# Optimization experiments

Hardware: AMD Instinct MI355X
Metric: run time of the kernel (lower is better)

Reference implementation:

```python
import jax, jax.numpy as jnp
from jax import lax
import numpy as np

EMBED = 20
FILTERS = 16
KSIZES = (1, 3, 5, 7, 9)
LIN_IN = 7 * len(KSIZES) * FILTERS  # 560
LIN_DIM = 64
SEQ_LENS = {'pep': 12, 'a1': 7, 'a2': 8, 'a3': 16, 'b1': 6, 'b2': 7, 'b3': 18}
BATCH = 16384


def setup_inputs() -> dict:
    key = jax.random.key(0)
    keys = jax.random.split(key, 16)
    inp = {}
    for i, (name, L) in enumerate(SEQ_LENS.items()):
        inp[name] = jax.random.normal(keys[i], (BATCH, EMBED, L), dtype=jnp.float32)
    # Conv weights: one stacked array per kernel size, [7 sequences, FILTERS, EMBED, k]
    for j, k in enumerate(KSIZES):
        inp[f'Wk{k}'] = jax.random.normal(keys[7 + j], (7, FILTERS, EMBED, k), dtype=jnp.float32) * 0.1
    inp['lin1_w'] = jax.random.normal(keys[12], (LIN_DIM, LIN_IN), dtype=jnp.float32) * 0.05
    inp['lin1_b'] = jnp.zeros((LIN_DIM,), dtype=jnp.float32)
    inp['lin2_w'] = jax.random.normal(keys[13], (1, LIN_DIM), dtype=jnp.float32) * 0.1
    inp['lin2_b'] = jnp.zeros((1,), dtype=jnp.float32)
    return inp


def _conv_relu_gmax(x, w):
    # x: [B, C, L], w: [F, C, k] -> SAME conv + ReLU + global max over length -> [B, F]
    y = lax.conv_general_dilated(x, w, window_strides=(1,), padding='SAME',
                                 dimension_numbers=('NCH', 'OIH', 'NCH'))
    return jnp.max(jax.nn.relu(y), axis=-1)


def _branch(x, ws):
    # x scaled by 1/5 as in the torch forward; concat pooled features over kernel sizes
    x = x / 5.0
    return jnp.concatenate([_conv_relu_gmax(x, w) for w in ws], axis=1)  # [B, 5*F]


def reference(pep, a1, a2, a3, b1, b2, b3, Wk1, Wk3, Wk5, Wk7, Wk9,
              lin1_w, lin1_b, lin2_w, lin2_b):
    seqs = [pep, a1, a2, a3, b1, b2, b3]
    Wks = [Wk1, Wk3, Wk5, Wk7, Wk9]
    feats = jnp.concatenate(
        [_branch(seqs[i], [W[i] for W in Wks]) for i in range(7)], axis=1)  # [B, 560]
    # Dropout is identity at inference.
    h = jax.nn.sigmoid(feats @ lin1_w.T + lin1_b)  # [B, 64]
    out = h @ lin2_w.T + lin2_b                    # [B, 1]
    return out.reshape(-1)                          # [B]
```

## Files before the change

### kernel.cpp

```cpp
#include <hip/hip_runtime.h>
#include <stdint.h>
#include <stddef.h>

typedef short bfrag __attribute__((ext_vector_type(8)));
typedef float f32x4 __attribute__((ext_vector_type(4)));

#define NSEQ 7

__constant__ int c_ks[5] = {1, 3, 5, 7, 9};

#define SLO0 3
#define SLO1 2
#define SLO2 1
#define SLO3 0
#define SLO4 0
#define SN0 1
#define SN1 3
#define SN2 5
#define SN3 6
#define SN4 7

#define XL_HW 22016
#define ZOFF 19200
#define PART_OFF 19456

static __device__ __forceinline__ unsigned short f2bf(float f) {
  unsigned int u = __float_as_uint(f);
  u += 0x7FFFu + ((u >> 16) & 1u);
  return (unsigned short)(u >> 16);
}

struct PrepArgs {
  const float* Wk[5];
  const float* lin1_w;
  bfrag* Wpack;
  bfrag* lin1pack;
};

__global__ __launch_bounds__(256) void prep_kernel(PrepArgs a) {
  int tid = blockIdx.x * 256 + threadIdx.x;
  const int NW = NSEQ * 5 * 7 * 64;
  if (tid < NW) {
    int lane = tid & 63, rest = tid >> 6;
    int step = rest % 7, nt = (rest / 7) % 5, seq = rest / 35;
    int quad = lane >> 4, f = lane & 15;
    int ks = c_ks[nt], off = (9 - ks) >> 1;
    const float* W = a.Wk[nt];
    bfrag s;
#pragma unroll
    for (int j = 0; j < 8; ++j) {
      int k = step * 32 + quad * 8 + j;
      int t = k / 24, c = k % 24;
      int tap = t - off;
      float val = 0.f;
      if (c < 20 && tap >= 0 && tap < ks)
        val = W[((seq * 16 + f) * 20 + c) * ks + tap] * 0.2f;
      s[j] = (short)f2bf(val);
    }
    a.Wpack[tid] = s;
  } else if (tid < NW + 4 * 18 * 64) {
    int t2 = tid - NW;
    int lane = t2 & 63, rest = t2 >> 6;
    int step = rest % 18, nt = rest / 18;
    int quad = lane >> 4, col = lane & 15;
    int n = nt * 16 + col;
    bfrag s;
#pragma unroll
    for (int j = 0; j < 8; ++j) {
      int k = step * 32 + quad * 8 + j;
      float val = (k < 560) ? a.lin1_w[n * 560 + k] : 0.f;
      s[j] = (short)f2bf(val);
    }
    a.lin1pack[t2] = s;
  }
}

struct ConvArgs {
  const float* x[NSEQ];
  const bfrag* Wpack;
  unsigned short* feats;
};

static __device__ __forceinline__ void store_feat(unsigned short* feats, int b, int k, float v) {
  int step = k >> 5, q = (k >> 3) & 3, j = k & 7;
  feats[((size_t)(b >> 4) * 18 + step) * 512 + (q * 16 + (b & 15)) * 8 + j] = f2bf(v);
}

template <int SLO, int SN>
static __device__ __forceinline__ void mfma_group(f32x4& acc, int s, const bfrag& Af,
                                                  const bfrag* BfBase) {
  if (s >= SLO && s < SLO + SN)
    acc = __builtin_amdgcn_mfma_f32_16x16x32_bf16(Af, BfBase[s - SLO], acc, 0, 0, 0);
}

static __device__ __forceinline__ void tile_mfma(const unsigned short* arow, const bfrag* Bf,
                                                 f32x4 acc[5]) {
#pragma unroll
  for (int s = 0; s < 7; ++s) {
    bfrag Af = *(const bfrag*)(arow + s * 32);
    mfma_group<SLO0, SN0>(acc[0], s, Af, Bf + 0);
    mfma_group<SLO1, SN1>(acc[1], s, Af, Bf + 1);
    mfma_group<SLO2, SN2>(acc[2], s, Af, Bf + 4);
    mfma_group<SLO3, SN3>(acc[3], s, Af, Bf + 9);
    acc[4] = __builtin_amdgcn_mfma_f32_16x16x32_bf16(Af, Bf[15 + s], acc[4], 0, 0, 0);
  }
}

template <int Lc, int SHIFTc, int SEQ6c, int TBBv, int Pv>
__device__ __forceinline__ void conv_body(unsigned short* xl, const ConvArgs& a,
                                          const int seq, const int b0) {
  const int tid = threadIdx.x;
  const float* xg = a.x[seq];

  constexpr int ZWORDS = (SEQ6c ? TBBv * Pv * 24 : ZOFF + 256) / 8;
  for (int i = tid; i < ZWORDS; i += 256) ((uint4*)xl)[i] = uint4{0, 0, 0, 0};
  __syncthreads();
  for (int r = tid; r < TBBv * 20; r += 256) {
    int b = r / 20, c = r % 20;
    const float* src = xg + ((size_t)(b0 + b) * 20 + c) * Lc;
    unsigned short* dst = xl + (b * Pv + 4) * 24 + c;
#pragma unroll
    for (int xi = 0; xi < Lc; ++xi) dst[xi * 24] = f2bf(src[xi]);
  }
  __syncthreads();

  const int wave = tid >> 6, lane = tid & 63, quad = lane >> 4, m = lane & 15;

  const bfrag* wp = a.Wpack + (size_t)(seq * 5 * 7) * 64 + lane;
  bfrag Bf[22];
  {
    int bi = 0;
#pragma unroll
    for (int i = 0; i < SN0; ++i) Bf[bi++] = wp[(0 * 7 + SLO0 + i) * 64];
#pragma unroll
    for (int i = 0; i < SN1; ++i) Bf[bi++] = wp[(1 * 7 + SLO1 + i) * 64];
#pragma unroll
    for (int i = 0; i < SN2; ++i) Bf[bi++] = wp[(2 * 7 + SLO2 + i) * 64];
#pragma unroll
    for (int i = 0; i < SN3; ++i) Bf[bi++] = wp[(3 * 7 + SLO3 + i) * 64];
#pragma unroll
    for (int i = 0; i < SN4; ++i) Bf[bi++] = wp[(4 * 7 + SLO4 + i) * 64];
  }

  float* part = (float*)(xl + PART_OFF);

  if (SEQ6c) {
    if (wave < 2) {
      int bl = wave * 8 + (m >> 1), l = 16 + (m & 1);
      const unsigned short* arow = &xl[(bl * Pv + l) * 24 + quad * 8];
      f32x4 acc[5];
#pragma unroll
      for (int g = 0; g < 5; ++g) acc[g] = f32x4{0.f, 0.f, 0.f, 0.f};
      tile_mfma(arow, Bf, acc);
#pragma unroll
      for (int g = 0; g < 5; ++g) {
        float p0 = fmaxf(fmaxf(acc[g][0], acc[g][1]), 0.f);
        float p1 = fmaxf(fmaxf(acc[g][2], acc[g][3]), 0.f);
        part[(wave * 8 + 2 * quad) * 80 + g * 16 + m] = p0;
        part[(wave * 8 + 2 * quad + 1) * 80 + g * 16 + m] = p1;
      }
    }
    __syncthreads();
  }

  constexpr int njobs = SEQ6c ? TBBv : ((TBBv << SHIFTc) >> 4);
  constexpr int bpt = (!SEQ6c && SHIFTc == 3) ? 2 : 1;
  constexpr int lmask = (1 << SHIFTc) - 1;

  for (int job = wave; job < njobs; job += 4) {
    int bl, l;
    if (SEQ6c) { bl = job; l = m; }
    else { int r = job * 16 + m; bl = r >> SHIFTc; l = r & lmask; }
    const unsigned short* arow = (SEQ6c || l < Lc)
        ? &xl[(bl * Pv + l) * 24 + quad * 8]
        : &xl[ZOFF + quad * 8];
    f32x4 acc[5];
#pragma unroll
    for (int g = 0; g < 5; ++g) acc[g] = f32x4{0.f, 0.f, 0.f, 0.f};
    tile_mfma(arow, Bf, acc);

    float v0 = fmaxf(fmaxf(fmaxf(acc[0][0], acc[0][1]), fmaxf(acc[0][2], acc[0][3])), 0.f);
    float v1 = fmaxf(fmaxf(fmaxf(acc[1][0], acc[1][1]), fmaxf(acc[1][2], acc[1][3])), 0.f);
    float v2 = fmaxf(fmaxf(fmaxf(acc[2][0], acc[2][1]), fmaxf(acc[2][2], acc[2][3])), 0.f);
    float v3 = fmaxf(fmaxf(fmaxf(acc[3][0], acc[3][1]), fmaxf(acc[3][2], acc[3][3])), 0.f);
    float v4 = fmaxf(fmaxf(fmaxf(acc[4][0], acc[4][1]), fmaxf(acc[4][2], acc[4][3])), 0.f);
    v0 = fmaxf(v0, __shfl_xor(v0, 16));
    v1 = fmaxf(v1, __shfl_xor(v1, 16));
    v2 = fmaxf(v2, __shfl_xor(v2, 16));
    v3 = fmaxf(v3, __shfl_xor(v3, 16));
    v4 = fmaxf(v4, __shfl_xor(v4, 16));
    if (bpt == 1) {
      v0 = fmaxf(v0, __shfl_xor(v0, 32));
      v1 = fmaxf(v1, __shfl_xor(v1, 32));
      v2 = fmaxf(v2, __shfl_xor(v2, 32));
      v3 = fmaxf(v3, __shfl_xor(v3, 32));
      v4 = fmaxf(v4, __shfl_xor(v4, 32));
      if (lane < 16) {
        if (SEQ6c) {
          v0 = fmaxf(v0, part[job * 80 + 0 + lane]);
          v1 = fmaxf(v1, part[job * 80 + 16 + lane]);
          v2 = fmaxf(v2, part[job * 80 + 32 + lane]);
          v3 = fmaxf(v3, part[job * 80 + 48 + lane]);
          v4 = fmaxf(v4, part[job * 80 + 64 + lane]);
        }
        int b = b0 + job, kb = seq * 80 + lane;
        store_feat(a.feats, b, kb, v0);      store_feat(a.feats, b, kb + 16, v1);
        store_feat(a.feats, b, kb + 32, v2); store_feat(a.feats, b, kb + 48, v3);
        store_feat(a.feats, b, kb + 64, v4);
      }
    } else {
      if ((lane & 16) == 0) {
        int b = b0 + job * 2 + (lane >> 5), kb = seq * 80 + (lane & 15);
        store_feat(a.feats, b, kb, v0);      store_feat(a.feats, b, kb + 16, v1);
        store_feat(a.feats, b, kb + 32, v2); store_feat(a.feats, b, kb + 48, v3);
        store_feat(a.feats, b, kb + 64, v4);
      }
    }
  }
}

__global__ __launch_bounds__(256, 3) void conv_kernel(ConvArgs a) {
  __shared__ __align__(16) unsigned short xl[XL_HW];
  const int bid = blockIdx.x;
  if (bid < 3072) {
    const int seq = bid >> 9, b0 = (bid & 511) * 32;
    switch (seq) {
      case 0: conv_body<12, 4, 0, 32, 25>(xl, a, 0, b0); break;
      case 1: conv_body< 7, 3, 0, 32, 25>(xl, a, 1, b0); break;
      case 2: conv_body< 8, 3, 0, 32, 25>(xl, a, 2, b0); break;
      case 3: conv_body<16, 4, 0, 32, 25>(xl, a, 3, b0); break;
      case 4: conv_body< 6, 3, 0, 32, 25>(xl, a, 4, b0); break;
      default: conv_body< 7, 3, 0, 32, 25>(xl, a, 5, b0); break;
    }
  } else {
    conv_body<18, 5, 1, 16, 41>(xl, a, 6, (bid - 3072) * 16);
  }
}

struct MlpArgs {
  const bfrag* feats;
  const bfrag* lin1pack;
  const float* lin1_b;
  const float* lin2_w;
  const float* lin2_b;
  float* out;
};

__global__ __launch_bounds__(256, 4) void mlp_kernel(MlpArgs a) {
  __shared__ float h[16 * 68];
  __shared__ float w2[64];
  const int tid = threadIdx.x;
  const int b0 = blockIdx.x * 16;
  if (tid < 64) w2[tid] = a.lin2_w[tid];
  const int wave = tid >> 6, lane = tid & 63, quad = lane >> 4, m = lane & 15;
  const int nt = wave;
  bfrag Bf[18];
#pragma unroll
  for (int s = 0; s < 18; ++s) Bf[s] = a.lin1pack[(nt * 18 + s) * 64 + lane];
  const bfrag* ap = a.feats + (size_t)blockIdx.x * 18 * 64 + lane;
  f32x4 acc = {0.f, 0.f, 0.f, 0.f};
#pragma unroll
  for (int s = 0; s < 18; ++s)
    acc = __builtin_amdgcn_mfma_f32_16x16x32_bf16(ap[s * 64], Bf[s], acc, 0, 0, 0);
  int n = nt * 16 + m;
  float bias = a.lin1_b[n];
#pragma unroll
  for (int r = 0; r < 4; ++r) {
    float pre = acc[r] + bias;
    h[(quad * 4 + r) * 68 + n] = 1.f / (1.f + __expf(-pre));
  }
  __syncthreads();
  int bl = tid >> 4, q = tid & 15;
  const float* hr = &h[bl * 68 + q * 4];
  float s = hr[0] * w2[q * 4] + hr[1] * w2[q * 4 + 1] + hr[2] * w2[q * 4 + 2] + hr[3] * w2[q * 4 + 3];
  s += __shfl_xor(s, 1);
  s += __shfl_xor(s, 2);
  s += __shfl_xor(s, 4);
  s += __shfl_xor(s, 8);
  if (q == 0) a.out[b0 + bl] = s + a.lin2_b[0];
}

extern "C" void kernel_launch(void* const* d_in, const int* in_sizes, int n_in,
                              void* d_out, int out_size, void* d_ws, size_t ws_size,
                              hipStream_t stream) {
  (void)in_sizes; (void)n_in; (void)out_size; (void)ws_size;
  char* ws = (char*)d_ws;
  bfrag* Wpack = (bfrag*)(ws + 0);
  bfrag* lin1pack = (bfrag*)(ws + 262144);
  unsigned short* feats = (unsigned short*)(ws + 393216);

  PrepArgs pa;
  for (int j = 0; j < 5; ++j) pa.Wk[j] = (const float*)d_in[7 + j];
  pa.lin1_w = (const float*)d_in[12];
  pa.Wpack = Wpack;
  pa.lin1pack = lin1pack;
  prep_kernel<<<80, 256, 0, stream>>>(pa);

  ConvArgs ca;
  for (int i = 0; i < NSEQ; ++i) ca.x[i] = (const float*)d_in[i];
  ca.Wpack = Wpack;
  ca.feats = feats;
  conv_kernel<<<4096, 256, 0, stream>>>(ca);

  MlpArgs ma;
  ma.feats = (const bfrag*)feats;
  ma.lin1pack = lin1pack;
  ma.lin1_b = (const float*)d_in[13];
  ma.lin2_w = (const float*)d_in[14];
  ma.lin2_b = (const float*)d_in[15];
  ma.out = (float*)d_out;
  mlp_kernel<<<1024, 256, 0, stream>>>(ma);
}
```

Baseline: 184.0 us.

## Pack conv rows densely across samples and reduce max via LDS atomics

Restructures the conv kernel so each block processes 16 samples of one sequence. Output rows are packed densely as sample*L+position, so MFMA tiles no longer waste lanes on padding positions up to a power of two. Per-sample global max pooling now uses integer atomicMax into an LDS buffer, replacing cross-lane shuffles. Each block then writes one vectorized bf16 store per feature chunk instead of scattered scalar stores. The smaller LDS footprint allows higher occupancy (launch bounds 4) and interleaves sequences across blocks; the cost is LDS atomic contention, more blocks, and a per-block reload of the weights.

```diff
diff --git a/kernel.cpp b/kernel.cpp
--- a/kernel.cpp
+++ b/kernel.cpp
@@ -20,9 +20,8 @@
 #define SN3 6
 #define SN4 7
 
-#define XL_HW 22016
-#define ZOFF 19200
-#define PART_OFF 19456
+#define STAGE_MAX_HW 10368
+#define XL_HW (STAGE_MAX_HW + 2560)
 
 static __device__ __forceinline__ unsigned short f2bf(float f) {
   unsigned int u = __float_as_uint(f);
@@ -81,11 +80,6 @@
   unsigned short* feats;
 };
 
-static __device__ __forceinline__ void store_feat(unsigned short* feats, int b, int k, float v) {
-  int step = k >> 5, q = (k >> 3) & 3, j = k & 7;
-  feats[((size_t)(b >> 4) * 18 + step) * 512 + (q * 16 + (b & 15)) * 8 + j] = f2bf(v);
-}
-
 template <int SLO, int SN>
 static __device__ __forceinline__ void mfma_group(f32x4& acc, int s, const bfrag& Af,
                                                   const bfrag* BfBase) {
@@ -106,21 +100,25 @@
   }
 }
 
-template <int Lc, int SHIFTc, int SEQ6c, int TBBv, int Pv>
+template <int L>
 __device__ __forceinline__ void conv_body(unsigned short* xl, const ConvArgs& a,
                                           const int seq, const int b0) {
+  constexpr int Pv = L + 9;
+  constexpr int SHW = Pv * 24;
+  constexpr int STAGE_HW = 16 * SHW;
+  int* pmax = (int*)(xl + STAGE_MAX_HW);
   const int tid = threadIdx.x;
   const float* xg = a.x[seq];
 
-  constexpr int ZWORDS = (SEQ6c ? TBBv * Pv * 24 : ZOFF + 256) / 8;
-  for (int i = tid; i < ZWORDS; i += 256) ((uint4*)xl)[i] = uint4{0, 0, 0, 0};
-  __syncthreads();
-  for (int r = tid; r < TBBv * 20; r += 256) {
+  for (int i = tid; i < STAGE_HW / 8; i += 256) ((uint4*)xl)[i] = uint4{0, 0, 0, 0};
+  for (int i = tid; i < 320; i += 256) ((uint4*)pmax)[i] = uint4{0, 0, 0, 0};
+  __syncthreads();
+  for (int r = tid; r < 16 * 20; r += 256) {
     int b = r / 20, c = r % 20;
-    const float* src = xg + ((size_t)(b0 + b) * 20 + c) * Lc;
-    unsigned short* dst = xl + (b * Pv + 4) * 24 + c;
-#pragma unroll
-    for (int xi = 0; xi < Lc; ++xi) dst[xi * 24] = f2bf(src[xi]);
+    const float* src = xg + ((size_t)(b0 + b) * 20 + c) * L;
+    unsigned short* dst = xl + b * SHW + 4 * 24 + c;
+#pragma unroll
+    for (int xi = 0; xi < L; ++xi) dst[xi * 24] = f2bf(src[xi]);
   }
   __syncthreads();
 
@@ -142,98 +140,71 @@
     for (int i = 0; i < SN4; ++i) Bf[bi++] = wp[(4 * 7 + SLO4 + i) * 64];
   }
 
-  float* part = (float*)(xl + PART_OFF);
-
-  if (SEQ6c) {
-    if (wave < 2) {
-      int bl = wave * 8 + (m >> 1), l = 16 + (m & 1);
-      const unsigned short* arow = &xl[(bl * Pv + l) * 24 + quad * 8];
-      f32x4 acc[5];
-#pragma unroll
-      for (int g = 0; g < 5; ++g) acc[g] = f32x4{0.f, 0.f, 0.f, 0.f};
-      tile_mfma(arow, Bf, acc);
-#pragma unroll
-      for (int g = 0; g < 5; ++g) {
-        float p0 = fmaxf(fmaxf(acc[g][0], acc[g][1]), 0.f);
-        float p1 = fmaxf(fmaxf(acc[g][2], acc[g][3]), 0.f);
-        part[(wave * 8 + 2 * quad) * 80 + g * 16 + m] = p0;
-        part[(wave * 8 + 2 * quad + 1) * 80 + g * 16 + m] = p1;
+  for (int tile = wave; tile < L; tile += 4) {
+    int r = tile * 16 + m;
+    int bl = r / L;
+    int l = r - bl * L;
+    const unsigned short* arow = &xl[bl * SHW + l * 24 + quad * 8];
+    f32x4 acc[5];
+#pragma unroll
+    for (int g = 0; g < 5; ++g) acc[g] = f32x4{0.f, 0.f, 0.f, 0.f};
+    tile_mfma(arow, Bf, acc);
+
+    int r0 = tile * 16 + quad * 4;
+    int s0 = r0 / L;
+    int l0 = r0 - s0 * L;
+    int base0 = s0 * 80 + m;
+#pragma unroll
+    for (int g = 0; g < 5; ++g) {
+      float v0 = fmaxf(acc[g][0], 0.f);
+      float v1 = fmaxf(acc[g][1], 0.f);
+      float v2 = fmaxf(acc[g][2], 0.f);
+      float v3 = fmaxf(acc[g][3], 0.f);
+      if constexpr ((L & 3) == 0) {
+        float va = fmaxf(fmaxf(v0, v1), fmaxf(v2, v3));
+        atomicMax(&pmax[base0 + g * 16], __float_as_int(va));
+      } else {
+        int cnt = L - l0;
+        float a1 = cnt > 1 ? v1 : 0.f, b1_ = cnt > 1 ? 0.f : v1;
+        float a2 = cnt > 2 ? v2 : 0.f, b2_ = cnt > 2 ? 0.f : v2;
+        float a3 = cnt > 3 ? v3 : 0.f, b3_ = cnt > 3 ? 0.f : v3;
+        float va = fmaxf(fmaxf(v0, a1), fmaxf(a2, a3));
+        atomicMax(&pmax[base0 + g * 16], __float_as_int(va));
+        if (cnt < 4) {
+          float vb = fmaxf(b1_, fmaxf(b2_, b3_));
+          atomicMax(&pmax[base0 + 80 + g * 16], __float_as_int(vb));
+        }
       }
     }
-    __syncthreads();
-  }
-
-  constexpr int njobs = SEQ6c ? TBBv : ((TBBv << SHIFTc) >> 4);
-  constexpr int bpt = (!SEQ6c && SHIFTc == 3) ? 2 : 1;
-  constexpr int lmask = (1 << SHIFTc) - 1;
-
-  for (int job = wave; job < njobs; job += 4) {
-    int bl, l;
-    if (SEQ6c) { bl = job; l = m; }
-    else { int r = job * 16 + m; bl = r >> SHIFTc; l = r & lmask; }
-    const unsigned short* arow = (SEQ6c || l < Lc)
-        ? &xl[(bl * Pv + l) * 24 + quad * 8]
-        : &xl[ZOFF + quad * 8];
-    f32x4 acc[5];
-#pragma unroll
-    for (int g = 0; g < 5; ++g) acc[g] = f32x4{0.f, 0.f, 0.f, 0.f};
-    tile_mfma(arow, Bf, acc);
-
-    float v0 = fmaxf(fmaxf(fmaxf(acc[0][0], acc[0][1]), fmaxf(acc[0][2], acc[0][3])), 0.f);
-    float v1 = fmaxf(fmaxf(fmaxf(acc[1][0], acc[1][1]), fmaxf(acc[1][2], acc[1][3])), 0.f);
-    float v2 = fmaxf(fmaxf(fmaxf(acc[2][0], acc[2][1]), fmaxf(acc[2][2], acc[2][3])), 0.f);
-    float v3 = fmaxf(fmaxf(fmaxf(acc[3][0], acc[3][1]), fmaxf(acc[3][2], acc[3][3])), 0.f);
-    float v4 = fmaxf(fmaxf(fmaxf(acc[4][0], acc[4][1]), fmaxf(acc[4][2], acc[4][3])), 0.f);
-    v0 = fmaxf(v0, __shfl_xor(v0, 16));
-    v1 = fmaxf(v1, __shfl_xor(v1, 16));
-    v2 = fmaxf(v2, __shfl_xor(v2, 16));
-    v3 = fmaxf(v3, __shfl_xor(v3, 16));
-    v4 = fmaxf(v4, __shfl_xor(v4, 16));
-    if (bpt == 1) {
-      v0 = fmaxf(v0, __shfl_xor(v0, 32));
-      v1 = fmaxf(v1, __shfl_xor(v1, 32));
-      v2 = fmaxf(v2, __shfl_xor(v2, 32));
-      v3 = fmaxf(v3, __shfl_xor(v3, 32));
-      v4 = fmaxf(v4, __shfl_xor(v4, 32));
-      if (lane < 16) {
-        if (SEQ6c) {
-          v0 = fmaxf(v0, part[job * 80 + 0 + lane]);
-          v1 = fmaxf(v1, part[job * 80 + 16 + lane]);
-          v2 = fmaxf(v2, part[job * 80 + 32 + lane]);
-          v3 = fmaxf(v3, part[job * 80 + 48 + lane]);
-          v4 = fmaxf(v4, part[job * 80 + 64 + lane]);
-        }
-        int b = b0 + job, kb = seq * 80 + lane;
-        store_feat(a.feats, b, kb, v0);      store_feat(a.feats, b, kb + 16, v1);
-        store_feat(a.feats, b, kb + 32, v2); store_feat(a.feats, b, kb + 48, v3);
-        store_feat(a.feats, b, kb + 64, v4);
-      }
-    } else {
-      if ((lane & 16) == 0) {
-        int b = b0 + job * 2 + (lane >> 5), kb = seq * 80 + (lane & 15);
-        store_feat(a.feats, b, kb, v0);      store_feat(a.feats, b, kb + 16, v1);
-        store_feat(a.feats, b, kb + 32, v2); store_feat(a.feats, b, kb + 48, v3);
-        store_feat(a.feats, b, kb + 64, v4);
-      }
-    }
-  }
-}
-
-__global__ __launch_bounds__(256, 3) void conv_kernel(ConvArgs a) {
+  }
+  __syncthreads();
+
+  if (tid < 160) {
+    int s = tid / 10, c = tid - (tid / 10) * 10;
+    int k0 = seq * 80 + c * 8;
+    bfrag outv;
+#pragma unroll
+    for (int j = 0; j < 8; ++j)
+      outv[j] = (short)f2bf(__int_as_float(pmax[s * 80 + c * 8 + j]));
+    int step = k0 >> 5, q = (k0 >> 3) & 3;
+    int b = b0 + s;
+    *(bfrag*)(a.feats + ((size_t)(b >> 4) * 18 + step) * 512 + (size_t)(q * 16 + (b & 15)) * 8) = outv;
+  }
+}
+
+__global__ __launch_bounds__(256, 4) void conv_kernel(ConvArgs a) {
   __shared__ __align__(16) unsigned short xl[XL_HW];
   const int bid = blockIdx.x;
-  if (bid < 3072) {
-    const int seq = bid >> 9, b0 = (bid & 511) * 32;
-    switch (seq) {
-      case 0: conv_body<12, 4, 0, 32, 25>(xl, a, 0, b0); break;
-      case 1: conv_body< 7, 3, 0, 32, 25>(xl, a, 1, b0); break;
-      case 2: conv_body< 8, 3, 0, 32, 25>(xl, a, 2, b0); break;
-      case 3: conv_body<16, 4, 0, 32, 25>(xl, a, 3, b0); break;
-      case 4: conv_body< 6, 3, 0, 32, 25>(xl, a, 4, b0); break;
-      default: conv_body< 7, 3, 0, 32, 25>(xl, a, 5, b0); break;
-    }
-  } else {
-    conv_body<18, 5, 1, 16, 41>(xl, a, 6, (bid - 3072) * 16);
+  const int seq = bid % 7;
+  const int b0 = (bid / 7) * 16;
+  switch (seq) {
+    case 0: conv_body<12>(xl, a, 0, b0); break;
+    case 1: conv_body< 7>(xl, a, 1, b0); break;
+    case 2: conv_body< 8>(xl, a, 2, b0); break;
+    case 3: conv_body<16>(xl, a, 3, b0); break;
+    case 4: conv_body< 6>(xl, a, 4, b0); break;
+    case 5: conv_body< 7>(xl, a, 5, b0); break;
+    default: conv_body<18>(xl, a, 6, b0); break;
   }
 }
 
@@ -300,7 +271,7 @@
   for (int i = 0; i < NSEQ; ++i) ca.x[i] = (const float*)d_in[i];
   ca.Wpack = Wpack;
   ca.feats = feats;
-  conv_kernel<<<4096, 256, 0, stream>>>(ca);
+  conv_kernel<<<7168, 256, 0, stream>>>(ca);
 
   MlpArgs ma;
   ma.feats = (const bfrag*)feats;
```

Result: no change. 182.2 us (-1.0%).
